# Kernel tuning notes

Hardware: AMD Instinct MI355X
Metric: run time of the kernel (lower is better)

Reference implementation:

```python
import jax, jax.numpy as jnp
import numpy as np

EMBED = 1024
HEADS = 16
HEAD = EMBED // HEADS
B, S = 8, 1024


def setup_inputs() -> dict:
    key = jax.random.key(0)
    ks = jax.random.split(key, 12)
    inp = {
        "values": jax.random.normal(ks[0], (B, S, EMBED), jnp.float32),
        "keys": jax.random.normal(ks[1], (B, S, EMBED), jnp.float32),
        "query": jax.random.normal(ks[2], (B, S, EMBED), jnp.float32),
        # causal mask broadcastable to [B, heads, q, k]
        "mask": jnp.broadcast_to(jnp.tril(jnp.ones((S, S), jnp.int32))[None, None], (B, 1, S, S)),
        "Wv": jax.random.normal(ks[3], (HEAD, HEAD), jnp.float32) / np.sqrt(HEAD),
        "bv": jnp.zeros((HEAD,), jnp.float32),
        "Wk": jax.random.normal(ks[4], (HEAD, HEAD), jnp.float32) / np.sqrt(HEAD),
        "bk": jnp.zeros((HEAD,), jnp.float32),
        "Wq": jax.random.normal(ks[5], (HEAD, HEAD), jnp.float32) / np.sqrt(HEAD),
        "bq": jnp.zeros((HEAD,), jnp.float32),
        "Wfc": jax.random.normal(ks[6], (EMBED, EMBED), jnp.float32) / np.sqrt(EMBED),
        "bfc": jnp.zeros((EMBED,), jnp.float32),
    }
    return inp


def reference(values, keys, query, mask, Wv, bv, Wk, bk, Wq, bq, Wfc, bfc):
    N, q_len = query.shape[0], query.shape[1]
    k_len, v_len = keys.shape[1], values.shape[1]
    # split heads: [N, S, H, D]
    v = values.reshape(N, v_len, HEADS, HEAD)
    k = keys.reshape(N, k_len, HEADS, HEAD)
    q = query.reshape(N, q_len, HEADS, HEAD)
    # per-head linear projections (torch Linear: x @ W.T + b)
    v = v @ Wv.T + bv
    k = k @ Wk.T + bk
    q = q @ Wq.T + bq
    # scores [N, H, q, k]
    scores = jnp.einsum('nqhz,nkhz->nhqk', q, k)
    scores = jnp.where(mask == 0, -jnp.inf, scores)
    # NOTE: original divides by sqrt(query_size) (sequence length), not head dim
    attn = jax.nn.softmax(scores / jnp.sqrt(jnp.float32(q_len)), axis=-1)
    out = jnp.einsum('nhqk,nkhz->nqhz', attn, v).reshape(N, q_len, HEADS * HEAD)
    return out @ Wfc.T + bfc
```

## Files before the change

### kernel.cpp

```cpp
#include <hip/hip_runtime.h>
#include <stdint.h>

typedef __attribute__((ext_vector_type(8))) short short8;
typedef __attribute__((ext_vector_type(4))) short short4v;
typedef __attribute__((ext_vector_type(4))) float floatx4;
typedef __attribute__((ext_vector_type(4))) unsigned short ushort4v;

#define HEADS 16
#define HEAD 64
#define SEQ 1024
#define BATCH 8

__device__ __forceinline__ unsigned short f2bf(float f) {
    union { float f; unsigned int u; } v; v.f = f;
    unsigned int r = v.u + 0x7FFFu + ((v.u >> 16) & 1u);
    return (unsigned short)(r >> 16);
}

__device__ __forceinline__ void gload_lds16(const void* g, void* l) {
    __builtin_amdgcn_global_load_lds((const __attribute__((address_space(1))) void*)g,
                                     (__attribute__((address_space(3))) void*)l, 16, 0, 0);
}

__global__ __launch_bounds__(256) void cvt_kernel(const float* __restrict__ in,
                                                  unsigned short* __restrict__ out) {
    int i = (blockIdx.x * 256 + threadIdx.x) * 4;
    float4 f = *(const float4*)(in + i);
    ushort4v v;
    v.x = f2bf(f.x); v.y = f2bf(f.y); v.z = f2bf(f.z); v.w = f2bf(f.w);
    *(ushort4v*)(out + i) = v;
}

__global__ __launch_bounds__(256, 3) void proj_kernel(
    const float* __restrict__ Vin, const float* __restrict__ Kin, const float* __restrict__ Qin,
    const float* __restrict__ Wv, const float* __restrict__ bv,
    const float* __restrict__ Wk, const float* __restrict__ bk,
    const float* __restrict__ Wq, const float* __restrict__ bq,
    unsigned short* __restrict__ q_ws, unsigned short* __restrict__ k_ws,
    unsigned short* __restrict__ v_ws)
{
    const int tid = threadIdx.x;
    const int tile = blockIdx.x;
    const int proj = blockIdx.y;

    const float* X; const float* W; const float* bias;
    if (proj == 0)      { X = Qin; W = Wq; bias = bq; }
    else if (proj == 1) { X = Kin; W = Wk; bias = bk; }
    else                { X = Vin; W = Wv; bias = bv; }

    __shared__ unsigned short sW[64 * 64];
    __shared__ unsigned short sE[4][32 * 72];

    const int wave = tid >> 6, lane = tid & 63;
    const int lq = lane & 15, quad = lane >> 4;
    const int m0 = tile * 32;
    const int b = m0 >> 10, s0 = m0 & 1023;

    const float qscale = 0.03125f * 1.44269504088896340736f;
    const float wscale = (proj == 0) ? qscale : 1.0f;

    {
        int n = tid >> 2, c0 = (tid & 3) * 16;
        const float* wr = W + n * 64 + c0;
#pragma unroll
        for (int half = 0; half < 2; ++half) {
            float4 fa = *(const float4*)(wr + half * 8);
            float4 fb = *(const float4*)(wr + half * 8 + 4);
            short8 v;
            v[0] = (short)f2bf(fa.x * wscale); v[1] = (short)f2bf(fa.y * wscale);
            v[2] = (short)f2bf(fa.z * wscale); v[3] = (short)f2bf(fa.w * wscale);
            v[4] = (short)f2bf(fb.x * wscale); v[5] = (short)f2bf(fb.y * wscale);
            v[6] = (short)f2bf(fb.z * wscale); v[7] = (short)f2bf(fb.w * wscale);
            int chunk = ((c0 >> 3) + half) ^ (n & 7);
            *(short8*)&sW[n * 64 + chunk * 8] = v;
        }
    }

    float biasv[4];
#pragma unroll
    for (int nt = 0; nt < 4; ++nt) biasv[nt] = bias[nt * 16 + lq] * wscale;

    __syncthreads();

    short8 bfr[2][4];
#pragma unroll
    for (int ks = 0; ks < 2; ++ks)
#pragma unroll
        for (int nt = 0; nt < 4; ++nt) {
            int n = nt * 16 + lq;
            bfr[ks][nt] = *(const short8*)&sW[n * 64 + (((quad + 4 * ks) ^ (n & 7)) * 8)];
        }

    const floatx4 zero4 = {0.f, 0.f, 0.f, 0.f};

    for (int hh = 0; hh < 4; ++hh) {
        const int h = wave * 4 + hh;

        short8 afr[2][2];
#pragma unroll
        for (int rg = 0; rg < 2; ++rg) {
            const float* xr = X + (size_t)(m0 + rg * 16 + lq) * 1024 + h * 64;
#pragma unroll
            for (int ks = 0; ks < 2; ++ks) {
                float4 f0 = *(const float4*)(xr + quad * 8 + ks * 32);
                float4 f1 = *(const float4*)(xr + quad * 8 + ks * 32 + 4);
                short8 a;
                a[0] = (short)f2bf(f0.x); a[1] = (short)f2bf(f0.y);
                a[2] = (short)f2bf(f0.z); a[3] = (short)f2bf(f0.w);
                a[4] = (short)f2bf(f1.x); a[5] = (short)f2bf(f1.y);
                a[6] = (short)f2bf(f1.z); a[7] = (short)f2bf(f1.w);
                afr[rg][ks] = a;
            }
        }

        floatx4 acc[2][4];
#pragma unroll
        for (int rg = 0; rg < 2; ++rg)
#pragma unroll
            for (int nt = 0; nt < 4; ++nt) acc[rg][nt] = zero4;
#pragma unroll
        for (int ks = 0; ks < 2; ++ks)
#pragma unroll
            for (int nt = 0; nt < 4; ++nt) {
                acc[0][nt] = __builtin_amdgcn_mfma_f32_16x16x32_bf16(afr[0][ks], bfr[ks][nt], acc[0][nt], 0, 0, 0);
                acc[1][nt] = __builtin_amdgcn_mfma_f32_16x16x32_bf16(afr[1][ks], bfr[ks][nt], acc[1][nt], 0, 0, 0);
            }

#pragma unroll
        for (int rg = 0; rg < 2; ++rg)
#pragma unroll
            for (int nt = 0; nt < 4; ++nt)
#pragma unroll
                for (int r = 0; r < 4; ++r)
                    sE[wave][(rg * 16 + quad * 4 + r) * 72 + nt * 16 + lq] =
                        f2bf(acc[rg][nt][r] + biasv[nt]);

        if (proj < 2) {
            unsigned short* dstb = (proj == 0 ? q_ws : k_ws);
#pragma unroll
            for (int r2 = 0; r2 < 2; ++r2) {
                int row = r2 * 16 + (lane >> 2), c = (lane & 3) * 16;
                const unsigned short* src = &sE[wave][row * 72 + c];
                unsigned short* dst = dstb + ((size_t)((b * 16 + h) * 1024 + s0 + row)) * 64 + c;
                *(short8*)dst = *(const short8*)src;
                *(short8*)(dst + 8) = *(const short8*)(src + 8);
            }
        } else {
            int d = lane;
            short8 v[4];
#pragma unroll
            for (int g = 0; g < 4; ++g)
#pragma unroll
                for (int j = 0; j < 8; ++j)
                    v[g][j] = (short)sE[wave][(g * 8 + j) * 72 + d];
            unsigned short* dst = v_ws + ((size_t)((b * 16 + h) * 64 + d)) * 1024 + s0;
#pragma unroll
            for (int g = 0; g < 4; ++g) *(short8*)(dst + g * 8) = v[g];
        }
    }
}

__global__ __launch_bounds__(256, 3) void attn_kernel(
    const unsigned short* __restrict__ q_ws, const unsigned short* __restrict__ k_ws,
    const unsigned short* __restrict__ v_ws, unsigned short* __restrict__ attn_ws)
{
    const int bh = blockIdx.x;
    const int b = bh >> 4, h = bh & 15;
    const int tid = threadIdx.x;
    const int wave = tid >> 6, lane = tid & 63;
    const int lq = lane & 15, quad = lane >> 4;
    const int r8 = lane >> 3, ch = lane & 7;
    const int sw = ch ^ r8;

    __shared__ unsigned short sK[64 * 64];
    __shared__ unsigned short sV[64 * 64];
    __shared__ unsigned short sP[4][32 * 64];

    const size_t head_off = (size_t)bh * SEQ * HEAD;
    const unsigned short* qb = q_ws + head_off;
    const unsigned short* kb = k_ws + head_off;
    const unsigned short* vb = v_ws + head_off;

    short8 ones;
#pragma unroll
    for (int j = 0; j < 8; ++j) ones[j] = (short)0x3F80;

    const floatx4 zero4 = {0.f, 0.f, 0.f, 0.f};

    for (int pass = 0; pass < 2; ++pass) {
        const int qt = pass ? (7 - blockIdx.y) : blockIdx.y;
        const int q0 = qt * 128;
        const int q_lo = q0 + wave * 32;
        const int q_hi = q_lo + 31;
        const int nkt = 2 * qt + 2;

        short8 aq[2][2];
#pragma unroll
        for (int rg = 0; rg < 2; ++rg) {
            const unsigned short* qp = qb + (size_t)(q0 + wave * 32 + rg * 16 + lq) * 64 + quad * 8;
            aq[rg][0] = *(const short8*)qp;
            aq[rg][1] = *(const short8*)(qp + 32);
        }

        floatx4 o[2][4];
        floatx4 lacc[2] = {zero4, zero4};
#pragma unroll
        for (int rg = 0; rg < 2; ++rg)
#pragma unroll
            for (int nt = 0; nt < 4; ++nt) o[rg][nt] = zero4;

        for (int kt = 0; kt < nkt; ++kt) {
#pragma unroll
            for (int i = 0; i < 2; ++i) {
                int br = wave * 16 + i * 8;
                const char* gK = (const char*)(kb + (size_t)(kt * 64 + br + r8) * 64) + sw * 16;
                gload_lds16(gK, (char*)sK + br * 128);
                const char* gV = (const char*)(vb + (size_t)(br + r8) * 1024 + kt * 64) + sw * 16;
                gload_lds16(gV, (char*)sV + br * 128);
            }
            __syncthreads();

            const bool skip = (kt * 64 > q_hi);
            if (!skip) {
                const bool full = (kt * 64 + 63 <= q_lo);

                floatx4 sT[2][4];
#pragma unroll
                for (int rg = 0; rg < 2; ++rg)
#pragma unroll
                    for (int nt = 0; nt < 4; ++nt) sT[rg][nt] = zero4;
#pragma unroll
                for (int ks = 0; ks < 2; ++ks) {
#pragma unroll
                    for (int nt = 0; nt < 4; ++nt) {
                        short8 kf = *(const short8*)(sK + (nt * 16 + lq) * 64 +
                                                     (((quad + 4 * ks) ^ (lq & 7)) * 8));
                        sT[0][nt] = __builtin_amdgcn_mfma_f32_16x16x32_bf16(kf, aq[0][ks], sT[0][nt], 0, 0, 0);
                        sT[1][nt] = __builtin_amdgcn_mfma_f32_16x16x32_bf16(kf, aq[1][ks], sT[1][nt], 0, 0, 0);
                    }
                }

                unsigned short* wp = &sP[wave][0];
#pragma unroll
                for (int rg = 0; rg < 2; ++rg) {
                    int q = q_lo + rg * 16 + lq;
#pragma unroll
                    for (int nt = 0; nt < 4; ++nt) {
                        int kcol0 = kt * 64 + nt * 16 + quad * 4;
                        short4v pk;
#pragma unroll
                        for (int r = 0; r < 4; ++r) {
                            float p = __builtin_amdgcn_exp2f(sT[rg][nt][r]);
                            if (!full && (kcol0 + r > q)) p = 0.f;
                            pk[r] = (short)f2bf(p);
                        }
                        *(short4v*)&wp[(rg * 16 + lq) * 64 +
                                       (((nt * 2 + (quad >> 1)) ^ (lq & 7)) * 8) + (quad & 1) * 4] = pk;
                    }
                }

                short8 vf[4][2];
#pragma unroll
                for (int nt = 0; nt < 4; ++nt)
#pragma unroll
                    for (int ks = 0; ks < 2; ++ks)
                        vf[nt][ks] = *(const short8*)(sV + (nt * 16 + lq) * 64 +
                                                      (((quad + 4 * ks) ^ (lq & 7)) * 8));
#pragma unroll
                for (int rg = 0; rg < 2; ++rg) {
#pragma unroll
                    for (int ks = 0; ks < 2; ++ks) {
                        short8 pa = *(const short8*)&sP[wave][(rg * 16 + lq) * 64 +
                                     (((ks * 4 + quad) ^ (lq & 7)) * 8)];
                        lacc[rg] = __builtin_amdgcn_mfma_f32_16x16x32_bf16(pa, ones, lacc[rg], 0, 0, 0);
#pragma unroll
                        for (int nt = 0; nt < 4; ++nt)
                            o[rg][nt] = __builtin_amdgcn_mfma_f32_16x16x32_bf16(pa, vf[nt][ks], o[rg][nt], 0, 0, 0);
                    }
                }
            }
            __syncthreads();
        }

#pragma unroll
        for (int rg = 0; rg < 2; ++rg) {
            float inv[4];
#pragma unroll
            for (int r = 0; r < 4; ++r) inv[r] = 1.f / lacc[rg][r];
            const int srow_base = q0 + wave * 32 + rg * 16 + quad * 4;
#pragma unroll
            for (int nt = 0; nt < 4; ++nt) {
                int col = h * 64 + nt * 16 + lq;
#pragma unroll
                for (int r = 0; r < 4; ++r) {
                    attn_ws[((size_t)(b * SEQ + srow_base + r)) * 1024 + col] = f2bf(o[rg][nt][r] * inv[r]);
                }
            }
        }
    }
}

__global__ __launch_bounds__(256) void fc_kernel(
    const unsigned short* __restrict__ A, const unsigned short* __restrict__ Bw,
    const float* __restrict__ bias, float* __restrict__ out)
{
    const int nt0 = blockIdx.x * 128;
    const int mt0 = blockIdx.y * 128;
    const int tid = threadIdx.x;
    const int wave = tid >> 6, lane = tid & 63;
    const int lq = lane & 15, quad = lane >> 4;
    const int wm = (wave >> 1) * 64, wn = (wave & 1) * 64;

    __shared__ unsigned short sA[128 * 32];
    __shared__ unsigned short sB[128 * 32];

    const floatx4 zero4 = {0.f, 0.f, 0.f, 0.f};
    floatx4 acc[4][4];
#pragma unroll
    for (int i = 0; i < 4; ++i)
#pragma unroll
        for (int j = 0; j < 4; ++j) acc[i][j] = zero4;

    for (int kt = 0; kt < 32; ++kt) {
#pragma unroll
        for (int issue = 0; issue < 2; ++issue) {
            int off = (issue * 4 + wave) * 1024 + lane * 16;
            int row = off >> 6;
            int cb = off & 63;
            const char* ga = (const char*)A + (size_t)(mt0 + row) * 2048 + kt * 64 + cb;
            gload_lds16(ga, (char*)sA + (issue * 4 + wave) * 1024);
            const char* gb = (const char*)Bw + (size_t)(nt0 + row) * 2048 + kt * 64 + cb;
            gload_lds16(gb, (char*)sB + (issue * 4 + wave) * 1024);
        }
        __syncthreads();

        short8 af[4], bf[4];
#pragma unroll
        for (int i = 0; i < 4; ++i) {
            af[i] = *(const short8*)(sA + (wm + i * 16 + lq) * 32 + quad * 8);
            bf[i] = *(const short8*)(sB + (wn + i * 16 + lq) * 32 + quad * 8);
        }
#pragma unroll
        for (int mi = 0; mi < 4; ++mi)
#pragma unroll
            for (int ni = 0; ni < 4; ++ni)
                acc[mi][ni] = __builtin_amdgcn_mfma_f32_16x16x32_bf16(af[mi], bf[ni], acc[mi][ni], 0, 0, 0);
        __syncthreads();
    }

#pragma unroll
    for (int mi = 0; mi < 4; ++mi) {
#pragma unroll
        for (int ni = 0; ni < 4; ++ni) {
            int col = nt0 + wn + ni * 16 + lq;
            float bc = bias[col];
#pragma unroll
            for (int r = 0; r < 4; ++r) {
                int row = mt0 + wm + mi * 16 + quad * 4 + r;
                out[(size_t)row * 1024 + col] = acc[mi][ni][r] + bc;
            }
        }
    }
}

extern "C" void kernel_launch(void* const* d_in, const int* in_sizes, int n_in,
                              void* d_out, int out_size, void* d_ws, size_t ws_size,
                              hipStream_t stream)
{
    const float* values = (const float*)d_in[0];
    const float* keys   = (const float*)d_in[1];
    const float* query  = (const float*)d_in[2];
    const float* Wv  = (const float*)d_in[4];
    const float* bv  = (const float*)d_in[5];
    const float* Wk  = (const float*)d_in[6];
    const float* bk  = (const float*)d_in[7];
    const float* Wq  = (const float*)d_in[8];
    const float* bq  = (const float*)d_in[9];
    const float* Wfc = (const float*)d_in[10];
    const float* bfc = (const float*)d_in[11];
    float* out = (float*)d_out;

    char* ws = (char*)d_ws;
    unsigned short* q_ws    = (unsigned short*)(ws);
    unsigned short* k_ws    = (unsigned short*)(ws + (16u << 20));
    unsigned short* v_ws    = (unsigned short*)(ws + (32u << 20));
    unsigned short* attn_ws = (unsigned short*)(ws + (48u << 20));
    unsigned short* wfc_ws  = (unsigned short*)(ws + (64u << 20));

    cvt_kernel<<<dim3(1024), dim3(256), 0, stream>>>(Wfc, wfc_ws);
    proj_kernel<<<dim3(256, 3), dim3(256), 0, stream>>>(
        values, keys, query, Wv, bv, Wk, bk, Wq, bq, q_ws, k_ws, v_ws);
    attn_kernel<<<dim3(128, 4), dim3(256), 0, stream>>>(q_ws, k_ws, v_ws, attn_ws);
    fc_kernel<<<dim3(8, 64), dim3(256), 0, stream>>>(attn_ws, wfc_ws, bfc, out);
}
```

Before: 252.8 us.

## Split projection kernel into smaller tiles and hoist input loads before weight setup

The projection kernel now handles 16 rows and 2 heads per wave instead of 32 rows and 4 heads, and the grid grows from 768 to 3072 blocks. All of a wave's input loads are issued up front, before the weight conversion and barrier, so global memory latency overlaps with the weight setup. The aim is more parallelism and memory-level concurrency in this bandwidth-bound pass over three 32 MB fp32 inputs. In exchange, each block redoes the weight load and bf16 conversion, so that work is repeated four times as often, and the V transpose stores become shorter 32-byte segments.

```diff
diff --git a/kernel.cpp b/kernel.cpp
--- a/kernel.cpp
+++ b/kernel.cpp
@@ -49,15 +49,28 @@
     else                { X = Vin; W = Wv; bias = bv; }
 
     __shared__ unsigned short sW[64 * 64];
-    __shared__ unsigned short sE[4][32 * 72];
+    __shared__ unsigned short sE[4][16 * 72];
 
     const int wave = tid >> 6, lane = tid & 63;
     const int lq = lane & 15, quad = lane >> 4;
-    const int m0 = tile * 32;
+    const int m0 = tile * 16;
     const int b = m0 >> 10, s0 = m0 & 1023;
+    const int h0 = blockIdx.z * 8 + wave * 2;
 
     const float qscale = 0.03125f * 1.44269504088896340736f;
     const float wscale = (proj == 0) ? qscale : 1.0f;
+
+    float4 raw[2][4];
+    {
+        const float* xr = X + (size_t)(m0 + lq) * 1024 + h0 * 64 + quad * 8;
+#pragma unroll
+        for (int hh = 0; hh < 2; ++hh)
+#pragma unroll
+            for (int ks = 0; ks < 2; ++ks) {
+                raw[hh][ks * 2 + 0] = *(const float4*)(xr + hh * 64 + ks * 32);
+                raw[hh][ks * 2 + 1] = *(const float4*)(xr + hh * 64 + ks * 32 + 4);
+            }
+    }
 
     {
         int n = tid >> 2, c0 = (tid & 3) * 16;
@@ -93,69 +106,54 @@
 
     const floatx4 zero4 = {0.f, 0.f, 0.f, 0.f};
 
-    for (int hh = 0; hh < 4; ++hh) {
-        const int h = wave * 4 + hh;
-
-        short8 afr[2][2];
-#pragma unroll
-        for (int rg = 0; rg < 2; ++rg) {
-            const float* xr = X + (size_t)(m0 + rg * 16 + lq) * 1024 + h * 64;
-#pragma unroll
-            for (int ks = 0; ks < 2; ++ks) {
-                float4 f0 = *(const float4*)(xr + quad * 8 + ks * 32);
-                float4 f1 = *(const float4*)(xr + quad * 8 + ks * 32 + 4);
-                short8 a;
-                a[0] = (short)f2bf(f0.x); a[1] = (short)f2bf(f0.y);
-                a[2] = (short)f2bf(f0.z); a[3] = (short)f2bf(f0.w);
-                a[4] = (short)f2bf(f1.x); a[5] = (short)f2bf(f1.y);
-                a[6] = (short)f2bf(f1.z); a[7] = (short)f2bf(f1.w);
-                afr[rg][ks] = a;
-            }
-        }
-
-        floatx4 acc[2][4];
-#pragma unroll
-        for (int rg = 0; rg < 2; ++rg)
-#pragma unroll
-            for (int nt = 0; nt < 4; ++nt) acc[rg][nt] = zero4;
+#pragma unroll
+    for (int hh = 0; hh < 2; ++hh) {
+        const int h = h0 + hh;
+
+        short8 afr[2];
+#pragma unroll
+        for (int ks = 0; ks < 2; ++ks) {
+            float4 f0 = raw[hh][ks * 2 + 0];
+            float4 f1 = raw[hh][ks * 2 + 1];
+            short8 a;
+            a[0] = (short)f2bf(f0.x); a[1] = (short)f2bf(f0.y);
+            a[2] = (short)f2bf(f0.z); a[3] = (short)f2bf(f0.w);
+            a[4] = (short)f2bf(f1.x); a[5] = (short)f2bf(f1.y);
+            a[6] = (short)f2bf(f1.z); a[7] = (short)f2bf(f1.w);
+            afr[ks] = a;
+        }
+
+        floatx4 acc[4] = {zero4, zero4, zero4, zero4};
 #pragma unroll
         for (int ks = 0; ks < 2; ++ks)
 #pragma unroll
-            for (int nt = 0; nt < 4; ++nt) {
-                acc[0][nt] = __builtin_amdgcn_mfma_f32_16x16x32_bf16(afr[0][ks], bfr[ks][nt], acc[0][nt], 0, 0, 0);
-                acc[1][nt] = __builtin_amdgcn_mfma_f32_16x16x32_bf16(afr[1][ks], bfr[ks][nt], acc[1][nt], 0, 0, 0);
-            }
-
-#pragma unroll
-        for (int rg = 0; rg < 2; ++rg)
-#pragma unroll
             for (int nt = 0; nt < 4; ++nt)
-#pragma unroll
-                for (int r = 0; r < 4; ++r)
-                    sE[wave][(rg * 16 + quad * 4 + r) * 72 + nt * 16 + lq] =
-                        f2bf(acc[rg][nt][r] + biasv[nt]);
+                acc[nt] = __builtin_amdgcn_mfma_f32_16x16x32_bf16(afr[ks], bfr[ks][nt], acc[nt], 0, 0, 0);
+
+#pragma unroll
+        for (int nt = 0; nt < 4; ++nt)
+#pragma unroll
+            for (int r = 0; r < 4; ++r)
+                sE[wave][(quad * 4 + r) * 72 + nt * 16 + lq] = f2bf(acc[nt][r] + biasv[nt]);
 
         if (proj < 2) {
             unsigned short* dstb = (proj == 0 ? q_ws : k_ws);
-#pragma unroll
-            for (int r2 = 0; r2 < 2; ++r2) {
-                int row = r2 * 16 + (lane >> 2), c = (lane & 3) * 16;
-                const unsigned short* src = &sE[wave][row * 72 + c];
-                unsigned short* dst = dstb + ((size_t)((b * 16 + h) * 1024 + s0 + row)) * 64 + c;
-                *(short8*)dst = *(const short8*)src;
-                *(short8*)(dst + 8) = *(const short8*)(src + 8);
-            }
+            int row = lane >> 2, c = (lane & 3) * 16;
+            const unsigned short* src = &sE[wave][row * 72 + c];
+            unsigned short* dst = dstb + ((size_t)((b * 16 + h) * 1024 + s0 + row)) * 64 + c;
+            *(short8*)dst = *(const short8*)src;
+            *(short8*)(dst + 8) = *(const short8*)(src + 8);
         } else {
             int d = lane;
-            short8 v[4];
-#pragma unroll
-            for (int g = 0; g < 4; ++g)
+            short8 v[2];
+#pragma unroll
+            for (int g = 0; g < 2; ++g)
 #pragma unroll
                 for (int j = 0; j < 8; ++j)
                     v[g][j] = (short)sE[wave][(g * 8 + j) * 72 + d];
             unsigned short* dst = v_ws + ((size_t)((b * 16 + h) * 64 + d)) * 1024 + s0;
-#pragma unroll
-            for (int g = 0; g < 4; ++g) *(short8*)(dst + g * 8) = v[g];
+            *(short8*)dst = v[0];
+            *(short8*)(dst + 8) = v[1];
         }
     }
 }
@@ -388,7 +386,7 @@
     unsigned short* wfc_ws  = (unsigned short*)(ws + (64u << 20));
 
     cvt_kernel<<<dim3(1024), dim3(256), 0, stream>>>(Wfc, wfc_ws);
-    proj_kernel<<<dim3(256, 3), dim3(256), 0, stream>>>(
+    proj_kernel<<<dim3(512, 3, 2), dim3(256), 0, stream>>>(
         values, keys, query, Wv, bv, Wk, bk, Wq, bq, q_ws, k_ws, v_ws);
     attn_kernel<<<dim3(128, 4), dim3(256), 0, stream>>>(q_ws, k_ws, v_ws, attn_ws);
     fc_kernel<<<dim3(8, 64), dim3(256), 0, stream>>>(attn_ws, wfc_ws, bfc, out);
```

Result: no change. 253.2 us (+0.2%).
